# Optimization experiments

Hardware: AMD Instinct MI355X
Metric: run time of the kernel (lower is better)

## Reference

```python
import jax, jax.numpy as jnp
import numpy as np

HEADS = 8

def _flatten(x, s1, s2):
    # 'b c (h s1) (w s2) -> b (h w) (s1 s2 c)'
    b, c, H, W = x.shape
    h, w = H // s1, W // s2
    x = x.reshape(b, c, h, s1, w, s2).transpose(0, 2, 4, 3, 5, 1)
    return x.reshape(b, h * w, s1 * s2 * c)

def _unflatten(x, h, w, s1, s2):
    # 'b (h w) (s1 s2 c) -> b c (h s1) (w s2)'
    b, n, e = x.shape
    c = e // (s1 * s2)
    x = x.reshape(b, h, w, s1, s2, c).transpose(0, 5, 1, 3, 2, 4)
    return x.reshape(b, c, h * s1, w * s2)

def _attn(x_detail, x_context, wq, bq, wk, bk, wv, bv, wo, bo):
    E = x_detail.shape[-1]
    d = E // HEADS
    scale = d ** -0.5
    def split(t):
        b, n, _ = t.shape
        return t.reshape(b, n, HEADS, d).transpose(0, 2, 1, 3)  # b h n d
    q = split(x_context @ wq.T + bq)
    k = split(x_detail @ wk.T + bk)
    v = split(x_detail @ wv.T + bv)
    att = jax.nn.softmax(jnp.einsum('bhqd,bhkd->bhqk', q, k) * scale, axis=-1)
    out = jnp.einsum('bhqk,bhkd->bhqd', att, v)
    b, h, n, _ = out.shape
    out = out.transpose(0, 2, 1, 3).reshape(b, n, E)
    return out @ wo.T + bo

def setup_inputs() -> dict:
    key = jax.random.key(0)
    ks = iter(jax.random.split(key, 64))
    inp = {}
    xshapes = [(16, 96, 56, 56), (16, 192, 28, 28), (16, 384, 14, 14), (16, 768, 7, 7)]
    names = ['x00', 'x10', 'x20', 'x30']
    for nm, sh in zip(names, xshapes):
        inp[nm + '_detail'] = jax.random.normal(next(ks), sh, dtype=jnp.float32)
        inp[nm + '_context'] = jax.random.normal(next(ks), sh, dtype=jnp.float32)
    embs = [384, 192, 384, 768]
    for i, E in enumerate(embs):
        for p in ['q', 'k', 'v', 'o']:
            inp[f'w{p}{i}'] = jax.random.normal(next(ks), (E, E), dtype=jnp.float32) * 0.02
            inp[f'b{p}{i}'] = jnp.zeros((E,), dtype=jnp.float32)
    return inp

def reference(x00_detail, x00_context, x10_detail, x10_context,
              x20_detail, x20_context, x30_detail, x30_context,
              wq0, bq0, wk0, bk0, wv0, bv0, wo0, bo0,
              wq1, bq1, wk1, bk1, wv1, bv1, wo1, bo1,
              wq2, bq2, wk2, bk2, wv2, bv2, wo2, bo2,
              wq3, bq3, wk3, bk3, wv3, bv3, wo3, bo3):
    # scale 0: 56x56 with 2x2 patching -> 784 tokens, emb 384
    o0 = x00_detail + _unflatten(
        _attn(_flatten(x00_detail, 2, 2), _flatten(x00_context, 2, 2),
              wq0, bq0, wk0, bk0, wv0, bv0, wo0, bo0), 28, 28, 2, 2)
    # scale 1: 28x28 -> 784 tokens, emb 192
    o1 = x10_detail + _unflatten(
        _attn(_flatten(x10_detail, 1, 1), _flatten(x10_context, 1, 1),
              wq1, bq1, wk1, bk1, wv1, bv1, wo1, bo1), 28, 28, 1, 1)
    # scale 2: 14x14 -> 196 tokens, emb 384
    o2 = x20_detail + _unflatten(
        _attn(_flatten(x20_detail, 1, 1), _flatten(x20_context, 1, 1),
              wq2, bq2, wk2, bk2, wv2, bv2, wo2, bo2), 14, 14, 1, 1)
    # scale 3: 7x7 -> 49 tokens, emb 768
    o3 = x30_detail + _unflatten(
        _attn(_flatten(x30_detail, 1, 1), _flatten(x30_context, 1, 1),
              wq3, bq3, wk3, bk3, wv3, bv3, wo3, bo3), 7, 7, 1, 1)
    return (o0, o1, o2, o3)
```

## Files before the change

### kernel.cpp

```cpp
#include <hip/hip_runtime.h>
#include <hip/hip_bf16.h>
#include <cstdint>
#include <cstddef>
#include <cmath>

typedef unsigned short bf16u;
typedef float f32x4 __attribute__((ext_vector_type(4)));
typedef short frag8 __attribute__((ext_vector_type(8)));

typedef __attribute__((address_space(1))) uint32_t u32g;
typedef __attribute__((address_space(3))) uint32_t u32l;

__device__ __forceinline__ void async_cp16(const bf16u* g, bf16u* l) {
    __builtin_amdgcn_global_load_lds((u32g*)g, (u32l*)l, 16, 0, 0);
}

__device__ __forceinline__ bf16u f2bf(float f) {
    union { float f; uint32_t u; } v; v.f = f;
    uint32_t u = v.u;
    return (bf16u)((u + 0x7fffu + ((u >> 16) & 1u)) >> 16);
}

__device__ __forceinline__ uint32_t pk2bf(float a, float b) {
    __hip_bfloat162 h = __float22bfloat162_rn(make_float2(a, b));
    union { __hip_bfloat162 h; uint32_t u; } c; c.h = h; return c.u;
}

__device__ __forceinline__ int vperm(int n) {
    return (n & ~63) | ((n & 15) << 2) | ((n >> 4) & 3);
}

static constexpr int cN[4]   = {784, 784, 196, 49};
static constexpr int cE[4]   = {384, 192, 384, 768};
static constexpr int cM[4]   = {12544, 12544, 3136, 784};
static constexpr int cC[4]   = {96, 192, 384, 768};
static constexpr int cH[4]   = {56, 28, 14, 7};
static constexpr int cS[4]   = {2, 1, 1, 1};
static constexpr int cWt[4]  = {28, 28, 14, 7};

static constexpr size_t xoff[4] = {0, 4816896, 7225344, 8429568};
static constexpr size_t voff[4] = {0, 6815744, 10223616, 12320768};
static constexpr size_t woff[4] = {0, 589824, 737280, 1327104};

__device__ __constant__ float qsc[4] = {0.20823509f, 0.29448888f, 0.20823509f, 0.14724444f};

static constexpr int qStart[13] = {0,294,588,882,957,1032,1107,1149,1191,1233,1821,2409,2997};
static constexpr int oStart[5]  = {0,294,369,411,999};

static constexpr int fStart[9] = {0,4800,9600,12000,14400,15744,17088,17856,18624};
static constexpr int wCum[17]  = {0,72,144,216,288,306,324,342,360,432,504,576,648,936,1224,1512,1800};
static constexpr int fNtn[4] = {25, 25, 7, 2};
static constexpr int fNtc[4] = {3, 6, 12, 24};
static constexpr int fSp[4]  = {4, 1, 1, 1};

struct BiasP { const float* p[16]; };
struct PrepP { const float* x[8]; const float* w[16]; };
struct OunfP { const float* xd[4]; };

__global__ __launch_bounds__(256) void prep(PrepP pp, bf16u* __restrict__ Xd,
                                            bf16u* __restrict__ Xc, bf16u* __restrict__ Wb) {
    int blk = blockIdx.x, tid = threadIdx.x;
    if (blk < 18624) {
        __shared__ float tile[32][33];
        int seg = 0;
        while (seg < 7 && blk >= fStart[seg + 1]) seg++;
        int s = seg >> 1, which = seg & 1;
        int l = blk - fStart[seg];
        int ntn = fNtn[s], ntc = fNtc[s], sp = fSp[s];
        int nt = l % ntn; l /= ntn;
        int ctl = l % ntc; l /= ntc;
        int spi = l % sp; int b = l / sp;
        int sv = cS[s];
        int s1i = spi / sv, s2i = spi % sv;
        int C = cC[s], H = cH[s], Wd = cH[s], N = cN[s], E2 = cE[s], Wt = cWt[s];
        const float* x = pp.x[s * 2 + which];
        bf16u* dst = (which ? Xc : Xd) + xoff[s];
        int tx = tid & 31, ty = tid >> 5;
        int n0 = nt * 32, c0 = ctl * 32;
#pragma unroll
        for (int rr = 0; rr < 4; ++rr) {
            int c = c0 + rr * 8 + ty;
            int n = n0 + tx;
            if (n < N) {
                int hh = (n / Wt) * sv + s1i;
                int ww = (n % Wt) * sv + s2i;
                tile[rr * 8 + ty][tx] = x[((size_t)(b * C + c) * H + hh) * Wd + ww];
            }
        }
        __syncthreads();
        int ebase = (s1i * sv + s2i) * C + c0;
#pragma unroll
        for (int rr = 0; rr < 4; ++rr) {
            int n = n0 + rr * 8 + ty;
            if (n < N)
                dst[((size_t)b * N + n) * E2 + ebase + tx] = f2bf(tile[tx][rr * 8 + ty]);
        }
    } else {
        int wb = blk - 18624;
        int m2 = 0;
        while (m2 < 15 && wb >= wCum[m2 + 1]) m2++;
        int s = m2 >> 2, mi = m2 & 3;
        size_t e2 = (size_t)cE[s] * cE[s];
        size_t base = (size_t)(wb - wCum[m2]) * 2048 + tid * 8;
        const float* src = pp.w[m2];
        bf16u* dst = Wb + woff[s] + mi * e2 + base;
        float4 a = *(const float4*)(src + base);
        float4 c = *(const float4*)(src + base + 4);
        bf16u o[8] = {f2bf(a.x), f2bf(a.y), f2bf(a.z), f2bf(a.w),
                      f2bf(c.x), f2bf(c.y), f2bf(c.z), f2bf(c.w)};
        *(frag8*)dst = *(frag8*)o;
    }
}

template<int MODE, int NN, int DHt, int DHPt, int NJt>
__device__ __forceinline__ void gemm_tile128(const bf16u* __restrict__ A, const bf16u* __restrict__ W,
                                             const float* __restrict__ bias,
                                             int M, int E, int mTile, int eTile, float oscale,
                                             bf16u* __restrict__ outB,
                                             bf16u* sm) {
    bf16u* A0 = sm;
    bf16u* B0 = sm + 4096;
    bf16u* A1 = sm + 8192;
    bf16u* B1 = sm + 12288;
    int tid = threadIdx.x, wave = tid >> 6, lane = tid & 63;
    int mbase = mTile * 128, ebase = eTile * 128;
    int wm = (wave & 1) * 64, wn = (wave >> 1) * 64;
    f32x4 acc[4][4] = {};
    int srow = tid >> 2, sch = (tid & 3) * 8;
    int K = E;
    int m0 = mbase + srow;      if (m0 >= M) m0 = M - 1;
    int m1 = mbase + srow + 64; if (m1 >= M) m1 = M - 1;
    const bf16u* Ag0 = A + (size_t)m0 * K + sch;
    const bf16u* Ag1 = A + (size_t)m1 * K + sch;
    const bf16u* Wg0 = W + (size_t)(ebase + srow) * K + sch;
    const bf16u* Wg1 = W + (size_t)(ebase + srow + 64) * K + sch;
    int la = (lane & 15) * 32 + (lane >> 4) * 8;

    auto stage = [&](int k0, bf16u* As, bf16u* Bs) {
        async_cp16(Ag0 + k0, As + tid * 8);
        async_cp16(Ag1 + k0, As + 2048 + tid * 8);
        async_cp16(Wg0 + k0, Bs + tid * 8);
        async_cp16(Wg1 + k0, Bs + 2048 + tid * 8);
    };
    auto compute = [&](const bf16u* As, const bf16u* Bs) {
        frag8 af[4], bfr[4];
#pragma unroll
        for (int i = 0; i < 4; ++i) {
            af[i]  = *(const frag8*)(As + (wm + i * 16) * 32 + la);
            bfr[i] = *(const frag8*)(Bs + (wn + i * 16) * 32 + la);
        }
#pragma unroll
        for (int i = 0; i < 4; ++i)
#pragma unroll
            for (int j = 0; j < 4; ++j)
                acc[i][j] = __builtin_amdgcn_mfma_f32_16x16x32_bf16(af[i], bfr[j], acc[i][j], 0, 0, 0);
    };

    stage(0, A0, B0);
    __syncthreads();
    for (int k0 = 0; k0 < K; k0 += 64) {
        stage(k0 + 32, A1, B1);
        compute(A0, B0);
        __syncthreads();
        if (k0 + 64 < K) stage(k0 + 64, A0, B0);
        compute(A1, B1);
        if (k0 + 64 < K) __syncthreads();
    }

#pragma unroll
    for (int mt = 0; mt < 4; ++mt) {
#pragma unroll
        for (int nt = 0; nt < 4; ++nt) {
            int col = ebase + wn + nt * 16 + (lane & 15);
            float bv = bias[col];
            int rbase = mbase + wm + mt * 16 + (lane >> 4) * 4;
#pragma unroll
            for (int r = 0; r < 4; ++r) {
                int rowg = rbase + r;
                if (rowg >= M) continue;
                float val = (acc[mt][nt][r] + bv) * oscale;
                if (MODE == 0) {
                    outB[(size_t)rowg * E + col] = f2bf(val);
                } else {
                    int bb2 = rowg / NN, n = rowg % NN;
                    int hh = col / DHt, d = col - hh * DHt;
                    outB[((size_t)(bb2 * 8 + hh) * DHPt + d) * NJt + vperm(n)] = f2bf(val);
                }
            }
        }
    }
}

template<int MODE, int NN, int DHt, int DHPt, int NJt>
__device__ __forceinline__ void gemm_tile64(const bf16u* __restrict__ A, const bf16u* __restrict__ W,
                                            const float* __restrict__ bias,
                                            int M, int E, int mTile, int eTile, float oscale,
                                            bf16u* __restrict__ outB,
                                            bf16u* sm) {
    bf16u* A0 = sm;
    bf16u* B0 = sm + 2048;
    bf16u* A1 = sm + 4096;
    bf16u* B1 = sm + 6144;
    int tid = threadIdx.x, wave = tid >> 6, lane = tid & 63;
    int mbase = mTile * 64, ebase = eTile * 64;
    int wm = (wave & 1) * 32, wn = (wave >> 1) * 32;
    f32x4 acc[2][2] = {};
    int srow = tid >> 2, sch = (tid & 3) * 8;
    int K = E;
    int m = mbase + srow; if (m >= M) m = M - 1;
    const bf16u* Ag = A + (size_t)m * K + sch;
    const bf16u* Wg = W + (size_t)(ebase + srow) * K + sch;
    int la = (lane & 15) * 32 + (lane >> 4) * 8;

    auto stage = [&](int k0, bf16u* As, bf16u* Bs) {
        async_cp16(Ag + k0, As + tid * 8);
        async_cp16(Wg + k0, Bs + tid * 8);
    };
    auto compute = [&](const bf16u* As, const bf16u* Bs) {
        frag8 af0 = *(const frag8*)(As + wm * 32 + la);
        frag8 af1 = *(const frag8*)(As + (wm + 16) * 32 + la);
        frag8 bf0 = *(const frag8*)(Bs + wn * 32 + la);
        frag8 bf1 = *(const frag8*)(Bs + (wn + 16) * 32 + la);
        acc[0][0] = __builtin_amdgcn_mfma_f32_16x16x32_bf16(af0, bf0, acc[0][0], 0, 0, 0);
        acc[0][1] = __builtin_amdgcn_mfma_f32_16x16x32_bf16(af0, bf1, acc[0][1], 0, 0, 0);
        acc[1][0] = __builtin_amdgcn_mfma_f32_16x16x32_bf16(af1, bf0, acc[1][0], 0, 0, 0);
        acc[1][1] = __builtin_amdgcn_mfma_f32_16x16x32_bf16(af1, bf1, acc[1][1], 0, 0, 0);
    };

    stage(0, A0, B0);
    __syncthreads();
    for (int k0 = 0; k0 < K; k0 += 64) {
        stage(k0 + 32, A1, B1);
        compute(A0, B0);
        __syncthreads();
        if (k0 + 64 < K) stage(k0 + 64, A0, B0);
        compute(A1, B1);
        if (k0 + 64 < K) __syncthreads();
    }

#pragma unroll
    for (int mt = 0; mt < 2; ++mt) {
#pragma unroll
        for (int nt = 0; nt < 2; ++nt) {
            int col = ebase + wn + nt * 16 + (lane & 15);
            float bv = bias[col];
            int rbase = mbase + wm + mt * 16 + (lane >> 4) * 4;
#pragma unroll
            for (int r = 0; r < 4; ++r) {
                int rowg = rbase + r;
                if (rowg >= M) continue;
                float val = (acc[mt][nt][r] + bv) * oscale;
                if (MODE == 0) {
                    outB[(size_t)rowg * E + col] = f2bf(val);
                } else {
                    int bb2 = rowg / NN, n = rowg % NN;
                    int hh = col / DHt, d = col - hh * DHt;
                    outB[((size_t)(bb2 * 8 + hh) * DHPt + d) * NJt + vperm(n)] = f2bf(val);
                }
            }
        }
    }
}

__global__ __launch_bounds__(256) void qkv_fat(const bf16u* __restrict__ Xd, const bf16u* __restrict__ Xc,
                                               const bf16u* __restrict__ Wb,
                                               bf16u* __restrict__ Qb, bf16u* __restrict__ Kb,
                                               bf16u* __restrict__ Vt, BiasP bp) {
    __shared__ __align__(16) bf16u sm[16384];
    int blk = blockIdx.x;
    int seg = 0;
    while (seg < 11 && blk >= qStart[seg + 1]) seg++;
    int t = blk - qStart[seg];
    if (seg < 9) {
        int s = (seg < 3) ? 0 : (seg < 6 ? 2 : 3);
        int op = seg % 3;
        int E = cE[s], M = cM[s];
        int ct = E >> 7;
        int mTile = t / ct, eTile = t - mTile * ct;
        const bf16u* A = (op == 0 ? Xc : Xd) + xoff[s];
        const bf16u* W = Wb + woff[s] + (size_t)op * E * E;
        const float* bias = bp.p[s * 4 + op];
        if (op == 2) {
            if (s == 0)
                gemm_tile128<1, 784, 48, 64, 832>(A, W, bias, M, E, mTile, eTile, 1.0f, Vt + voff[0], sm);
            else if (s == 2)
                gemm_tile128<1, 196, 48, 64, 256>(A, W, bias, M, E, mTile, eTile, 1.0f, Vt + voff[2], sm);
            else
                gemm_tile128<1, 49, 96, 96, 64>(A, W, bias, M, E, mTile, eTile, 1.0f, Vt + voff[3], sm);
        } else {
            float osc = (op == 0) ? qsc[s] : 1.0f;
            bf16u* outB = (op == 0 ? Qb : Kb) + xoff[s];
            gemm_tile128<0, 0, 1, 0, 0>(A, W, bias, M, E, mTile, eTile, osc, outB, sm);
        }
    } else {
        int op = seg - 9;
        int E = 192, M = 12544;
        int mTile = t / 3, eTile = t - mTile * 3;
        const bf16u* A = (op == 0 ? Xc : Xd) + xoff[1];
        const bf16u* W = Wb + woff[1] + (size_t)op * E * E;
        const float* bias = bp.p[4 + op];
        if (op == 2)
            gemm_tile64<1, 784, 24, 32, 832>(A, W, bias, M, E, mTile, eTile, 1.0f, Vt + voff[1], sm);
        else {
            float osc = (op == 0) ? qsc[1] : 1.0f;
            bf16u* outB = (op == 0 ? Qb : Kb) + xoff[1];
            gemm_tile64<0, 0, 1, 0, 0>(A, W, bias, M, E, mTile, eTile, osc, outB, sm);
        }
    }
}

__device__ __forceinline__ f32x4 bfly_add16(f32x4 v) {
#pragma unroll
    for (int m = 1; m <= 8; m <<= 1) {
        f32x4 o;
#pragma unroll
        for (int e = 0; e < 4; ++e) o[e] = __shfl_xor(v[e], m);
#pragma unroll
        for (int e = 0; e < 4; ++e) v[e] += o[e];
    }
    return v;
}

template<int DH, int N>
__device__ __forceinline__ void attn_body2(bf16u* __restrict__ smem,
                                           const bf16u* __restrict__ Q, const bf16u* __restrict__ K,
                                           const bf16u* __restrict__ Vt, bf16u* __restrict__ O,
                                           int lin) {
    constexpr int DHP = (DH == 24) ? 32 : 64;
    constexpr int C8  = DHP / 8;
    constexpr int CM  = C8 - 1;
    constexpr int KC  = DHP / 32;
    constexpr int DHT = (DH + 15) / 16;
    constexpr int VR  = DHT * 16;
    constexpr int NT  = (N + 63) / 64;
    constexpr int NJc = NT * 64;
    constexpr int E   = DH * 8;
    constexpr int KS  = 64 * C8;
    constexpr int TS  = KS + VR * 8;
    constexpr int RND = (TS + 255) / 256;
    constexpr int PP  = 72;

    bf16u* buf0 = smem;
    bf16u* buf1 = smem + (size_t)TS * 8;
    bf16u* Ps   = smem + (size_t)2 * TS * 8;

    const int qt = lin % NT;
    const int r2 = lin / NT;
    const int h = r2 & 7, b = r2 >> 3;
    const int qb = qt * 64;
    const int tid = threadIdx.x, wave = tid >> 6, lane = tid & 63;
    const int mrow = lane & 15, quad = lane >> 4;

    const bf16u* Kb2 = K + (size_t)b * N * E + h * DH;
    const bf16u* Vb2 = Vt + (size_t)(b * 8 + h) * DHP * NJc;

    auto stage = [&](int jt, bf16u* buf) {
#pragma unroll
        for (int r = 0; r < RND; ++r) {
            int s = tid + r * 256;
            bf16u* dst = buf + (size_t)s * 8;
            if (s < KS) {
                int row = s / C8;
                int cl = (s & CM) ^ (row & CM);
                int n = jt * 64 + row; if (n >= N) n = N - 1;
                async_cp16(Kb2 + (size_t)n * E + cl * 8, dst);
            } else if (s < TS) {
                int v = s - KS;
                int d = v >> 3;
                int cl = (v & 7) ^ (d & 7);
                async_cp16(Vb2 + (size_t)d * NJc + jt * 64 + cl * 8, dst);
            }
        }
    };

    stage(0, buf0);

    frag8 qf[KC];
    {
        int qn = qb + wave * 16 + mrow; if (qn >= N) qn = N - 1;
        const bf16u* qp = Q + (size_t)(b * N + qn) * E + h * DH;
#pragma unroll
        for (int kc = 0; kc < KC; ++kc) {
            int col = kc * 32 + quad * 8;
            frag8 v = {};
            if (col < DH) v = *(const frag8*)(qp + col);
            qf[kc] = v;
        }
    }

    f32x4 lrun = {0.f, 0.f, 0.f, 0.f};
    f32x4 oacc[DHT];
#pragma unroll
    for (int t = 0; t < DHT; ++t) oacc[t] = f32x4{0.f, 0.f, 0.f, 0.f};

    bf16u* Pw = Ps + wave * 16 * PP;

    __syncthreads();

    int p = 0;
    for (int jt = 0; jt < NT; ++jt) {
        bf16u* KsB = p ? buf1 : buf0;
        bf16u* VsB = KsB + (size_t)KS * 8;
        if (jt + 1 < NT) stage(jt + 1, p ? buf0 : buf1);

        f32x4 s[4];
        const bool domask = ((N & 63) != 0) && (jt == NT - 1);
#pragma unroll
        for (int sub = 0; sub < 4; ++sub) {
            f32x4 acc = {};
#pragma unroll
            for (int kc = 0; kc < KC; ++kc) {
                int c = kc * 4 + quad;
                frag8 bfr = *(const frag8*)(KsB + ((size_t)((sub * 16 + mrow) * C8 + (c ^ (mrow & CM)))) * 8);
                acc = __builtin_amdgcn_mfma_f32_16x16x32_bf16(qf[kc], bfr, acc, 0, 0, 0);
            }
            if (domask) {
                int col = jt * 64 + sub * 16 + mrow;
                if (col >= N) { acc[0] = acc[1] = acc[2] = acc[3] = -30000.f; }
            }
            s[sub] = acc;
        }

#pragma unroll
        for (int sub = 0; sub < 4; ++sub)
#pragma unroll
            for (int e = 0; e < 4; ++e) {
                float px = __builtin_amdgcn_exp2f(s[sub][e]);
                s[sub][e] = px;
                lrun[e] += px;
            }

#pragma unroll
        for (int e = 0; e < 4; ++e) {
            uint2 u;
            u.x = pk2bf(s[0][e], s[1][e]);
            u.y = pk2bf(s[2][e], s[3][e]);
            *(uint2*)(Pw + (quad * 4 + e) * PP + mrow * 4) = u;
        }

#pragma unroll
        for (int jc = 0; jc < 2; ++jc) {
            frag8 af = *(const frag8*)(Pw + mrow * PP + jc * 32 + quad * 8);
            int c = jc * 4 + quad;
#pragma unroll
            for (int t = 0; t < DHT; ++t) {
                frag8 bfr = *(const frag8*)(VsB + ((size_t)((t * 16 + mrow) * 8 + (c ^ (mrow & 7)))) * 8);
                oacc[t] = __builtin_amdgcn_mfma_f32_16x16x32_bf16(af, bfr, oacc[t], 0, 0, 0);
            }
        }
        __syncthreads();
        p ^= 1;
    }

    lrun = bfly_add16(lrun);
    f32x4 linv;
#pragma unroll
    for (int e = 0; e < 4; ++e) linv[e] = 1.0f / lrun[e];
#pragma unroll
    for (int t = 0; t < DHT; ++t) {
        int d = t * 16 + mrow;
        if (d >= DH) continue;
#pragma unroll
        for (int e = 0; e < 4; ++e) {
            int n = qb + wave * 16 + quad * 4 + e;
            if (n < N)
                O[((size_t)(b * N + n)) * E + h * DH + d] = f2bf(oacc[t][e] * linv[e]);
        }
    }
}

__global__ __launch_bounds__(256, 4) void attn_fat(const bf16u* __restrict__ Qb, const bf16u* __restrict__ Kb,
                                                   const bf16u* __restrict__ Vt, bf16u* __restrict__ Ob) {
    __shared__ __align__(16) bf16u smem[18944];
    int blk = blockIdx.x;
    if (blk < 1664)
        attn_body2<48, 784>(smem, Qb + xoff[0], Kb + xoff[0], Vt + voff[0], Ob + xoff[0], blk);
    else if (blk < 3328)
        attn_body2<24, 784>(smem, Qb + xoff[1], Kb + xoff[1], Vt + voff[1], Ob + xoff[1], blk - 1664);
    else
        attn_body2<48, 196>(smem, Qb + xoff[2], Kb + xoff[2], Vt + voff[2], Ob + xoff[2], blk - 3328);
}

__global__ __launch_bounds__(256, 2) void attn_s3(const bf16u* __restrict__ Qg, const bf16u* __restrict__ Kg,
                                                  const bf16u* __restrict__ Vtg, bf16u* __restrict__ Og) {
    constexpr int DH = 96, N = 49, DHP = 96, KC = 3, DHT = 6, NJc = 64, E = 768;
    constexpr int KP = 104, QP = 104, VP = 72, PP = 72, C8 = 12;
    __shared__ __align__(16) bf16u smem[20224];
    bf16u* Ks = smem;
    bf16u* Vs = Ks + 64 * KP;
    bf16u* QsPw = Vs + DHT * 16 * VP;

    const bf16u* Q = Qg + xoff[3];
    const bf16u* K = Kg + xoff[3];
    const bf16u* Vt = Vtg + voff[3];
    bf16u* O = Og + xoff[3];

    int lin = blockIdx.x;
    int h = lin & 7, b = lin >> 3;
    int tid = threadIdx.x, wave = tid >> 6, lane = tid & 63;
    int mrow = lane & 15, quad = lane >> 4;

    for (int idx = tid; idx < 64 * C8; idx += 256) {
        int row = idx / C8, col = (idx % C8) * 8;
        int n = row; if (n >= N) n = N - 1;
        frag8 v = {};
        if (col < DH) v = *(const frag8*)(Q + ((size_t)(b * N + n)) * E + h * DH + col);
        *(frag8*)(QsPw + row * QP + col) = v;
    }
    for (int idx = tid; idx < 64 * C8; idx += 256) {
        int row = idx / C8, col = (idx % C8) * 8;
        int n = row; if (n >= N) n = N - 1;
        frag8 v = {};
        if (col < DH) v = *(const frag8*)(K + (size_t)(b * N + n) * E + h * DH + col);
        *(frag8*)(Ks + row * KP + col) = v;
    }
    const bf16u* Vb2 = Vt + (size_t)(b * 8 + h) * DHP * NJc;
    for (int idx = tid; idx < DHT * 16 * 8; idx += 256) {
        int d = idx / 8, j = (idx % 8) * 8;
        frag8 v = {};
        if (d < DH) v = *(const frag8*)(Vb2 + (size_t)d * NJc + j);
        *(frag8*)(Vs + d * VP + j) = v;
    }
    __syncthreads();
    frag8 qf[KC];
#pragma unroll
    for (int kc = 0; kc < KC; ++kc)
        qf[kc] = *(const frag8*)(QsPw + (wave * 16 + mrow) * QP + kc * 32 + quad * 8);
    __syncthreads();
    bf16u* Pw = QsPw + wave * 16 * PP;

    f32x4 lrun = {0.f, 0.f, 0.f, 0.f};
    f32x4 oacc[DHT];
#pragma unroll
    for (int t = 0; t < DHT; ++t) oacc[t] = f32x4{0.f, 0.f, 0.f, 0.f};

    f32x4 s[4];
#pragma unroll
    for (int sub = 0; sub < 4; ++sub) {
        f32x4 acc = {};
#pragma unroll
        for (int kc = 0; kc < KC; ++kc) {
            frag8 bfr = *(const frag8*)(Ks + (sub * 16 + mrow) * KP + kc * 32 + quad * 8);
            acc = __builtin_amdgcn_mfma_f32_16x16x32_bf16(qf[kc], bfr, acc, 0, 0, 0);
        }
        int col = sub * 16 + mrow;
        if (col >= N) { acc[0] = acc[1] = acc[2] = acc[3] = -30000.f; }
        s[sub] = acc;
    }
#pragma unroll
    for (int sub = 0; sub < 4; ++sub)
#pragma unroll
        for (int e = 0; e < 4; ++e) {
            float px = __builtin_amdgcn_exp2f(s[sub][e]);
            s[sub][e] = px;
            lrun[e] += px;
        }
#pragma unroll
    for (int e = 0; e < 4; ++e) {
        uint2 u;
        u.x = pk2bf(s[0][e], s[1][e]);
        u.y = pk2bf(s[2][e], s[3][e]);
        *(uint2*)(Pw + (quad * 4 + e) * PP + mrow * 4) = u;
    }
#pragma unroll
    for (int jc = 0; jc < 2; ++jc) {
        frag8 af = *(const frag8*)(Pw + mrow * PP + jc * 32 + quad * 8);
#pragma unroll
        for (int t = 0; t < DHT; ++t) {
            frag8 bfr = *(const frag8*)(Vs + (t * 16 + mrow) * VP + jc * 32 + quad * 8);
            oacc[t] = __builtin_amdgcn_mfma_f32_16x16x32_bf16(af, bfr, oacc[t], 0, 0, 0);
        }
    }

    lrun = bfly_add16(lrun);
    f32x4 linv;
#pragma unroll
    for (int e = 0; e < 4; ++e) linv[e] = 1.0f / lrun[e];
#pragma unroll
    for (int t = 0; t < DHT; ++t) {
        int d = t * 16 + mrow;
#pragma unroll
        for (int e = 0; e < 4; ++e) {
            int n = wave * 16 + quad * 4 + e;
            if (n < N)
                O[((size_t)(b * N + n)) * E + h * DH + d] = f2bf(oacc[t][e] * linv[e]);
        }
    }
}

template<int SC>
__device__ __forceinline__ size_t out_index(int rowg, int cg) {
    if (SC == 0) {
        int b = rowg / 784, n = rowg - b * 784;
        int slot = cg / 96, c = cg - slot * 96;
        int hh = n / 28, ww = n - hh * 28;
        return ((size_t)(b * 96 + c) * 56 + 2 * hh + (slot >> 1)) * 56 + 2 * ww + (slot & 1);
    } else if (SC == 1) {
        int b = rowg / 784, n = rowg - b * 784;
        return ((size_t)(b * 192 + cg)) * 784 + n;
    } else if (SC == 2) {
        int b = rowg / 196, n = rowg - b * 196;
        return ((size_t)(b * 384 + cg)) * 196 + n;
    } else {
        int b = rowg / 49, n = rowg - b * 49;
        return ((size_t)(b * 768 + cg)) * 49 + n;
    }
}

template<int SC>
__device__ __forceinline__ void o_tile128(const bf16u* __restrict__ A, const bf16u* __restrict__ W,
                                          const float* __restrict__ bias,
                                          const float* __restrict__ xd, float* __restrict__ out,
                                          int M, int E, int mTile, int eTile, bf16u* sm) {
    bf16u* A0 = sm;
    bf16u* B0 = sm + 4096;
    bf16u* A1 = sm + 8192;
    bf16u* B1 = sm + 12288;
    int tid = threadIdx.x, wave = tid >> 6, lane = tid & 63;
    int mbase = mTile * 128, ebase = eTile * 128;
    int wm = (wave & 1) * 64, wn = (wave >> 1) * 64;
    int mrow = lane & 15, quad = lane >> 4;
    f32x4 acc[4][4] = {};
    int srow = tid >> 2, sch = (tid & 3) * 8;
    int K = E;
    int m0 = mbase + srow;      if (m0 >= M) m0 = M - 1;
    int m1 = mbase + srow + 64; if (m1 >= M) m1 = M - 1;
    const bf16u* Ag0 = A + (size_t)m0 * K + sch;
    const bf16u* Ag1 = A + (size_t)m1 * K + sch;
    const bf16u* Wg0 = W + (size_t)(ebase + srow) * K + sch;
    const bf16u* Wg1 = W + (size_t)(ebase + srow + 64) * K + sch;
    int la = mrow * 32 + quad * 8;

    auto stage = [&](int k0, bf16u* As, bf16u* Bs) {
        async_cp16(Ag0 + k0, As + tid * 8);
        async_cp16(Ag1 + k0, As + 2048 + tid * 8);
        async_cp16(Wg0 + k0, Bs + tid * 8);
        async_cp16(Wg1 + k0, Bs + 2048 + tid * 8);
    };
    auto compute = [&](const bf16u* As, const bf16u* Bs) {
        frag8 af[4], bfr[4];
#pragma unroll
        for (int i = 0; i < 4; ++i) {
            af[i]  = *(const frag8*)(As + (wm + i * 16) * 32 + la);
            bfr[i] = *(const frag8*)(Bs + (wn + i * 16) * 32 + la);
        }
#pragma unroll
        for (int i = 0; i < 4; ++i)
#pragma unroll
            for (int j = 0; j < 4; ++j)
                acc[i][j] = __builtin_amdgcn_mfma_f32_16x16x32_bf16(af[i], bfr[j], acc[i][j], 0, 0, 0);
    };

    stage(0, A0, B0);
    __syncthreads();
    for (int k0 = 0; k0 < K; k0 += 64) {
        stage(k0 + 32, A1, B1);
        compute(A0, B0);
        __syncthreads();
        if (k0 + 64 < K) stage(k0 + 64, A0, B0);
        compute(A1, B1);
        if (k0 + 64 < K) __syncthreads();
    }

    float* Ls = (float*)sm;
#pragma unroll
    for (int ph = 0; ph < 4; ++ph) {
        __syncthreads();
        if ((wave & 1) == (ph >> 1)) {
            int mt0 = (ph & 1) * 2;
#pragma unroll
            for (int mi = 0; mi < 2; ++mi) {
                int mt = mt0 + mi;
#pragma unroll
                for (int nt = 0; nt < 4; ++nt)
#pragma unroll
                    for (int r = 0; r < 4; ++r)
                        Ls[(mi * 16 + quad * 4 + r) * 133 + wn + nt * 16 + mrow] = acc[mt][nt][r];
            }
        }
        __syncthreads();
        int rb = mbase + ph * 32;
#pragma unroll
        for (int i = 0; i < 16; ++i) {
            int coll = (tid >> 5) + i * 8;
            int l = tid & 31;
            int rg = rb + l;
            if (rg < M) {
                int cg = ebase + coll;
                size_t oi = out_index<SC>(rg, cg);
                out[oi] = xd[oi] + Ls[l * 133 + coll] + bias[cg];
            }
        }
    }
}

__device__ __forceinline__ void o_tile64_s1(const bf16u* __restrict__ A, const bf16u* __restrict__ W,
                                            const float* __restrict__ bias,
                                            const float* __restrict__ xd, float* __restrict__ out,
                                            int M, int E, int mTile, int eTile, bf16u* sm) {
    bf16u* A0 = sm;
    bf16u* B0 = sm + 2048;
    bf16u* A1 = sm + 4096;
    bf16u* B1 = sm + 6144;
    int tid = threadIdx.x, wave = tid >> 6, lane = tid & 63;
    int mbase = mTile * 64, ebase = eTile * 64;
    int wm = (wave & 1) * 32, wn = (wave >> 1) * 32;
    int mrow = lane & 15, quad = lane >> 4;
    f32x4 acc[2][2] = {};
    int srow = tid >> 2, sch = (tid & 3) * 8;
    int K = E;
    int m = mbase + srow; if (m >= M) m = M - 1;
    const bf16u* Ag = A + (size_t)m * K + sch;
    const bf16u* Wg = W + (size_t)(ebase + srow) * K + sch;
    int la = mrow * 32 + quad * 8;

    auto stage = [&](int k0, bf16u* As, bf16u* Bs) {
        async_cp16(Ag + k0, As + tid * 8);
        async_cp16(Wg + k0, Bs + tid * 8);
    };
    auto compute = [&](const bf16u* As, const bf16u* Bs) {
        frag8 af0 = *(const frag8*)(As + wm * 32 + la);
        frag8 af1 = *(const frag8*)(As + (wm + 16) * 32 + la);
        frag8 bf0 = *(const frag8*)(Bs + wn * 32 + la);
        frag8 bf1 = *(const frag8*)(Bs + (wn + 16) * 32 + la);
        acc[0][0] = __builtin_amdgcn_mfma_f32_16x16x32_bf16(af0, bf0, acc[0][0], 0, 0, 0);
        acc[0][1] = __builtin_amdgcn_mfma_f32_16x16x32_bf16(af0, bf1, acc[0][1], 0, 0, 0);
        acc[1][0] = __builtin_amdgcn_mfma_f32_16x16x32_bf16(af1, bf0, acc[1][0], 0, 0, 0);
        acc[1][1] = __builtin_amdgcn_mfma_f32_16x16x32_bf16(af1, bf1, acc[1][1], 0, 0, 0);
    };

    stage(0, A0, B0);
    __syncthreads();
    for (int k0 = 0; k0 < K; k0 += 64) {
        stage(k0 + 32, A1, B1);
        compute(A0, B0);
        __syncthreads();
        if (k0 + 64 < K) stage(k0 + 64, A0, B0);
        compute(A1, B1);
        if (k0 + 64 < K) __syncthreads();
    }

    float* Ls = (float*)sm;
#pragma unroll
    for (int ph = 0; ph < 2; ++ph) {
        __syncthreads();
        if ((wave & 1) == ph) {
#pragma unroll
            for (int mt = 0; mt < 2; ++mt)
#pragma unroll
                for (int nt = 0; nt < 2; ++nt)
#pragma unroll
                    for (int r = 0; r < 4; ++r)
                        Ls[(mt * 16 + quad * 4 + r) * 69 + wn + nt * 16 + mrow] = acc[mt][nt][r];
        }
        __syncthreads();
        int rb = mbase + ph * 32;
#pragma unroll
        for (int i = 0; i < 8; ++i) {
            int coll = (tid >> 5) + i * 8;
            int l = tid & 31;
            int rg = rb + l;
            if (rg < M) {
                int cg = ebase + coll;
                size_t oi = out_index<1>(rg, cg);
                out[oi] = xd[oi] + Ls[l * 69 + coll] + bias[cg];
            }
        }
    }
}

__global__ __launch_bounds__(256) void ounf_fat(const bf16u* __restrict__ Ob, const bf16u* __restrict__ Wb,
                                                float* __restrict__ out, BiasP bp, OunfP up) {
    __shared__ __align__(16) bf16u sm[16384];
    int blk = blockIdx.x;
    int seg = 0;
    while (seg < 3 && blk >= oStart[seg + 1]) seg++;
    int t = blk - oStart[seg];
    if (seg < 3) {
        int s = (seg == 0) ? 0 : (seg == 1 ? 2 : 3);
        int E = cE[s], M = cM[s];
        int ct = E >> 7;
        int mTile = t / ct, eTile = t - mTile * ct;
        const bf16u* A = Ob + xoff[s];
        const bf16u* W = Wb + woff[s] + (size_t)3 * E * E;
        if (s == 0)
            o_tile128<0>(A, W, bp.p[3], up.xd[0], out + xoff[0], M, E, mTile, eTile, sm);
        else if (s == 2)
            o_tile128<2>(A, W, bp.p[11], up.xd[2], out + xoff[2], M, E, mTile, eTile, sm);
        else
            o_tile128<3>(A, W, bp.p[15], up.xd[3], out + xoff[3], M, E, mTile, eTile, sm);
    } else {
        int E = 192, M = 12544;
        int mTile = t / 3, eTile = t - mTile * 3;
        o_tile64_s1(Ob + xoff[1], Wb + woff[1] + (size_t)3 * E * E, bp.p[7],
                    up.xd[1], out + xoff[1], M, E, mTile, eTile, sm);
    }
}

extern "C" void kernel_launch(void* const* d_in, const int* in_sizes, int n_in,
                              void* d_out, int out_size, void* d_ws, size_t ws_size,
                              hipStream_t stream) {
    bf16u* ws = (bf16u*)d_ws;
    bf16u* Qb = ws;
    bf16u* Kb = ws + 9031680;
    bf16u* Vt = ws + 18063360;
    bf16u* Ob = ws + 31170560;
    bf16u* Wb = ws + 40202240;
    bf16u* Xd = ws + 43888640;
    bf16u* Xc = ws + 52920320;
    float* out = (float*)d_out;

    PrepP pp; BiasP bb; OunfP ux;
    for (int s = 0; s < 4; ++s) {
        pp.x[s * 2]     = (const float*)d_in[s * 2];
        pp.x[s * 2 + 1] = (const float*)d_in[s * 2 + 1];
        ux.xd[s]        = (const float*)d_in[s * 2];
        int w0 = 8 + s * 8;
        pp.w[s * 4 + 0] = (const float*)d_in[w0 + 0];
        pp.w[s * 4 + 1] = (const float*)d_in[w0 + 2];
        pp.w[s * 4 + 2] = (const float*)d_in[w0 + 4];
        pp.w[s * 4 + 3] = (const float*)d_in[w0 + 6];
        bb.p[s * 4 + 0] = (const float*)d_in[w0 + 1];
        bb.p[s * 4 + 1] = (const float*)d_in[w0 + 3];
        bb.p[s * 4 + 2] = (const float*)d_in[w0 + 5];
        bb.p[s * 4 + 3] = (const float*)d_in[w0 + 7];
    }

    prep<<<20424, 256, 0, stream>>>(pp, Xd, Xc, Wb);
    qkv_fat<<<2997, 256, 0, stream>>>(Xd, Xc, Wb, Qb, Kb, Vt, bb);
    attn_fat<<<3840, 256, 0, stream>>>(Qb, Kb, Vt, Ob);
    attn_s3<<<128, 256, 0, stream>>>(Qb, Kb, Vt, Ob);
    ounf_fat<<<999, 256, 0, stream>>>(Ob, Wb, out, bb, ux);
}
```

Baseline: 375.9 us.

## Fuse K and V projections into one GEMM sharing the detail-input tile

Splits the combined QKV launch into a Q-only kernel and a fused K/V kernel. The K/V kernel loads each detail-activation tile once and multiplies it against both Wk and Wv, keeping two accumulator sets. This halves the activation reads for the K and V projections. In exchange it doubles accumulator registers per block, raises LDS use to 48KB, adds a second launch, and caps occupancy at two blocks per CU.

```diff
diff --git a/kernel.cpp b/kernel.cpp
--- a/kernel.cpp
+++ b/kernel.cpp
@@ -44,7 +44,7 @@
 
 __device__ __constant__ float qsc[4] = {0.20823509f, 0.29448888f, 0.20823509f, 0.14724444f};
 
-static constexpr int qStart[13] = {0,294,588,882,957,1032,1107,1149,1191,1233,1821,2409,2997};
+static constexpr int qStartQ[5] = {0, 294, 369, 411, 999};
 static constexpr int oStart[5]  = {0,294,369,411,999};
 
 static constexpr int fStart[9] = {0,4800,9600,12000,14400,15744,17088,17856,18624};
@@ -262,50 +262,221 @@
     }
 }
 
-__global__ __launch_bounds__(256) void qkv_fat(const bf16u* __restrict__ Xd, const bf16u* __restrict__ Xc,
-                                               const bf16u* __restrict__ Wb,
-                                               bf16u* __restrict__ Qb, bf16u* __restrict__ Kb,
-                                               bf16u* __restrict__ Vt, BiasP bp) {
+template<int NN, int DHt, int DHPt, int NJt>
+__device__ __forceinline__ void gemm_kv128(const bf16u* __restrict__ A, const bf16u* __restrict__ Wk,
+                                           const bf16u* __restrict__ Wv,
+                                           const float* __restrict__ bk, const float* __restrict__ bv,
+                                           int M, int E, int mTile, int eTile,
+                                           bf16u* __restrict__ Ko, bf16u* __restrict__ Vo, bf16u* sm) {
+    bf16u* A0 = sm;           bf16u* K0 = sm + 4096;   bf16u* V0 = sm + 8192;
+    bf16u* A1 = sm + 12288;   bf16u* K1 = sm + 16384;  bf16u* V1 = sm + 20480;
+    int tid = threadIdx.x, wave = tid >> 6, lane = tid & 63;
+    int mbase = mTile * 128, ebase = eTile * 128;
+    int wm = (wave & 1) * 64, wn = (wave >> 1) * 64;
+    f32x4 acck[4][4] = {};
+    f32x4 accv[4][4] = {};
+    int srow = tid >> 2, sch = (tid & 3) * 8;
+    int Kd = E;
+    int m0 = mbase + srow;      if (m0 >= M) m0 = M - 1;
+    int m1 = mbase + srow + 64; if (m1 >= M) m1 = M - 1;
+    const bf16u* Ag0 = A + (size_t)m0 * Kd + sch;
+    const bf16u* Ag1 = A + (size_t)m1 * Kd + sch;
+    const bf16u* Kg0 = Wk + (size_t)(ebase + srow) * Kd + sch;
+    const bf16u* Kg1 = Wk + (size_t)(ebase + srow + 64) * Kd + sch;
+    const bf16u* Vg0 = Wv + (size_t)(ebase + srow) * Kd + sch;
+    const bf16u* Vg1 = Wv + (size_t)(ebase + srow + 64) * Kd + sch;
+    int la = (lane & 15) * 32 + (lane >> 4) * 8;
+
+    auto stage = [&](int k0, bf16u* As, bf16u* Ks, bf16u* Vs) {
+        async_cp16(Ag0 + k0, As + tid * 8);
+        async_cp16(Ag1 + k0, As + 2048 + tid * 8);
+        async_cp16(Kg0 + k0, Ks + tid * 8);
+        async_cp16(Kg1 + k0, Ks + 2048 + tid * 8);
+        async_cp16(Vg0 + k0, Vs + tid * 8);
+        async_cp16(Vg1 + k0, Vs + 2048 + tid * 8);
+    };
+    auto compute = [&](const bf16u* As, const bf16u* Ks, const bf16u* Vs) {
+        frag8 af[4], bfr[4];
+#pragma unroll
+        for (int i = 0; i < 4; ++i)
+            af[i] = *(const frag8*)(As + (wm + i * 16) * 32 + la);
+#pragma unroll
+        for (int i = 0; i < 4; ++i)
+            bfr[i] = *(const frag8*)(Ks + (wn + i * 16) * 32 + la);
+#pragma unroll
+        for (int i = 0; i < 4; ++i)
+#pragma unroll
+            for (int j = 0; j < 4; ++j)
+                acck[i][j] = __builtin_amdgcn_mfma_f32_16x16x32_bf16(af[i], bfr[j], acck[i][j], 0, 0, 0);
+#pragma unroll
+        for (int i = 0; i < 4; ++i)
+            bfr[i] = *(const frag8*)(Vs + (wn + i * 16) * 32 + la);
+#pragma unroll
+        for (int i = 0; i < 4; ++i)
+#pragma unroll
+            for (int j = 0; j < 4; ++j)
+                accv[i][j] = __builtin_amdgcn_mfma_f32_16x16x32_bf16(af[i], bfr[j], accv[i][j], 0, 0, 0);
+    };
+
+    stage(0, A0, K0, V0);
+    __syncthreads();
+    for (int k0 = 0; k0 < Kd; k0 += 64) {
+        stage(k0 + 32, A1, K1, V1);
+        compute(A0, K0, V0);
+        __syncthreads();
+        if (k0 + 64 < Kd) stage(k0 + 64, A0, K0, V0);
+        compute(A1, K1, V1);
+        if (k0 + 64 < Kd) __syncthreads();
+    }
+
+#pragma unroll
+    for (int mt = 0; mt < 4; ++mt) {
+#pragma unroll
+        for (int nt = 0; nt < 4; ++nt) {
+            int col = ebase + wn + nt * 16 + (lane & 15);
+            float bkc = bk[col];
+            float bvc = bv[col];
+            int hh = col / DHt, d = col - hh * DHt;
+            int rbase = mbase + wm + mt * 16 + (lane >> 4) * 4;
+#pragma unroll
+            for (int r = 0; r < 4; ++r) {
+                int rowg = rbase + r;
+                if (rowg >= M) continue;
+                Ko[(size_t)rowg * E + col] = f2bf(acck[mt][nt][r] + bkc);
+                int bb2 = rowg / NN, n = rowg % NN;
+                Vo[((size_t)(bb2 * 8 + hh) * DHPt + d) * NJt + vperm(n)] = f2bf(accv[mt][nt][r] + bvc);
+            }
+        }
+    }
+}
+
+template<int NN, int DHt, int DHPt, int NJt>
+__device__ __forceinline__ void gemm_kv64(const bf16u* __restrict__ A, const bf16u* __restrict__ Wk,
+                                          const bf16u* __restrict__ Wv,
+                                          const float* __restrict__ bk, const float* __restrict__ bv,
+                                          int M, int E, int mTile, int eTile,
+                                          bf16u* __restrict__ Ko, bf16u* __restrict__ Vo, bf16u* sm) {
+    bf16u* A0 = sm;          bf16u* K0 = sm + 2048;  bf16u* V0 = sm + 4096;
+    bf16u* A1 = sm + 6144;   bf16u* K1 = sm + 8192;  bf16u* V1 = sm + 10240;
+    int tid = threadIdx.x, wave = tid >> 6, lane = tid & 63;
+    int mbase = mTile * 64, ebase = eTile * 64;
+    int wm = (wave & 1) * 32, wn = (wave >> 1) * 32;
+    f32x4 acck[2][2] = {};
+    f32x4 accv[2][2] = {};
+    int srow = tid >> 2, sch = (tid & 3) * 8;
+    int Kd = E;
+    int m = mbase + srow; if (m >= M) m = M - 1;
+    const bf16u* Ag = A + (size_t)m * Kd + sch;
+    const bf16u* Kg = Wk + (size_t)(ebase + srow) * Kd + sch;
+    const bf16u* Vg = Wv + (size_t)(ebase + srow) * Kd + sch;
+    int la = (lane & 15) * 32 + (lane >> 4) * 8;
+
+    auto stage = [&](int k0, bf16u* As, bf16u* Ks, bf16u* Vs) {
+        async_cp16(Ag + k0, As + tid * 8);
+        async_cp16(Kg + k0, Ks + tid * 8);
+        async_cp16(Vg + k0, Vs + tid * 8);
+    };
+    auto compute = [&](const bf16u* As, const bf16u* Ks, const bf16u* Vs) {
+        frag8 af0 = *(const frag8*)(As + wm * 32 + la);
+        frag8 af1 = *(const frag8*)(As + (wm + 16) * 32 + la);
+        frag8 k0f = *(const frag8*)(Ks + wn * 32 + la);
+        frag8 k1f = *(const frag8*)(Ks + (wn + 16) * 32 + la);
+        acck[0][0] = __builtin_amdgcn_mfma_f32_16x16x32_bf16(af0, k0f, acck[0][0], 0, 0, 0);
+        acck[0][1] = __builtin_amdgcn_mfma_f32_16x16x32_bf16(af0, k1f, acck[0][1], 0, 0, 0);
+        acck[1][0] = __builtin_amdgcn_mfma_f32_16x16x32_bf16(af1, k0f, acck[1][0], 0, 0, 0);
+        acck[1][1] = __builtin_amdgcn_mfma_f32_16x16x32_bf16(af1, k1f, acck[1][1], 0, 0, 0);
+        frag8 v0f = *(const frag8*)(Vs + wn * 32 + la);
+        frag8 v1f = *(const frag8*)(Vs + (wn + 16) * 32 + la);
+        accv[0][0] = __builtin_amdgcn_mfma_f32_16x16x32_bf16(af0, v0f, accv[0][0], 0, 0, 0);
+        accv[0][1] = __builtin_amdgcn_mfma_f32_16x16x32_bf16(af0, v1f, accv[0][1], 0, 0, 0);
+        accv[1][0] = __builtin_amdgcn_mfma_f32_16x16x32_bf16(af1, v0f, accv[1][0], 0, 0, 0);
+        accv[1][1] = __builtin_amdgcn_mfma_f32_16x16x32_bf16(af1, v1f, accv[1][1], 0, 0, 0);
+    };
+
+    stage(0, A0, K0, V0);
+    __syncthreads();
+    for (int k0 = 0; k0 < Kd; k0 += 64) {
+        stage(k0 + 32, A1, K1, V1);
+        compute(A0, K0, V0);
+        __syncthreads();
+        if (k0 + 64 < Kd) stage(k0 + 64, A0, K0, V0);
+        compute(A1, K1, V1);
+        if (k0 + 64 < Kd) __syncthreads();
+    }
+
+#pragma unroll
+    for (int mt = 0; mt < 2; ++mt) {
+#pragma unroll
+        for (int nt = 0; nt < 2; ++nt) {
+            int col = ebase + wn + nt * 16 + (lane & 15);
+            float bkc = bk[col];
+            float bvc = bv[col];
+            int hh = col / DHt, d = col - hh * DHt;
+            int rbase = mbase + wm + mt * 16 + (lane >> 4) * 4;
+#pragma unroll
+            for (int r = 0; r < 4; ++r) {
+                int rowg = rbase + r;
+                if (rowg >= M) continue;
+                Ko[(size_t)rowg * E + col] = f2bf(acck[mt][nt][r] + bkc);
+                int bb2 = rowg / NN, n = rowg % NN;
+                Vo[((size_t)(bb2 * 8 + hh) * DHPt + d) * NJt + vperm(n)] = f2bf(accv[mt][nt][r] + bvc);
+            }
+        }
+    }
+}
+
+__global__ __launch_bounds__(256) void qkv_q(const bf16u* __restrict__ Xc, const bf16u* __restrict__ Wb,
+                                             bf16u* __restrict__ Qb, BiasP bp) {
     __shared__ __align__(16) bf16u sm[16384];
     int blk = blockIdx.x;
     int seg = 0;
-    while (seg < 11 && blk >= qStart[seg + 1]) seg++;
-    int t = blk - qStart[seg];
-    if (seg < 9) {
-        int s = (seg < 3) ? 0 : (seg < 6 ? 2 : 3);
-        int op = seg % 3;
+    while (seg < 3 && blk >= qStartQ[seg + 1]) seg++;
+    int t = blk - qStartQ[seg];
+    if (seg < 3) {
+        int s = (seg == 0) ? 0 : (seg == 1 ? 2 : 3);
         int E = cE[s], M = cM[s];
         int ct = E >> 7;
         int mTile = t / ct, eTile = t - mTile * ct;
-        const bf16u* A = (op == 0 ? Xc : Xd) + xoff[s];
-        const bf16u* W = Wb + woff[s] + (size_t)op * E * E;
-        const float* bias = bp.p[s * 4 + op];
-        if (op == 2) {
-            if (s == 0)
-                gemm_tile128<1, 784, 48, 64, 832>(A, W, bias, M, E, mTile, eTile, 1.0f, Vt + voff[0], sm);
-            else if (s == 2)
-                gemm_tile128<1, 196, 48, 64, 256>(A, W, bias, M, E, mTile, eTile, 1.0f, Vt + voff[2], sm);
-            else
-                gemm_tile128<1, 49, 96, 96, 64>(A, W, bias, M, E, mTile, eTile, 1.0f, Vt + voff[3], sm);
-        } else {
-            float osc = (op == 0) ? qsc[s] : 1.0f;
-            bf16u* outB = (op == 0 ? Qb : Kb) + xoff[s];
-            gemm_tile128<0, 0, 1, 0, 0>(A, W, bias, M, E, mTile, eTile, osc, outB, sm);
-        }
+        gemm_tile128<0, 0, 1, 0, 0>(Xc + xoff[s], Wb + woff[s], bp.p[s * 4], M, E, mTile, eTile,
+                                    qsc[s], Qb + xoff[s], sm);
     } else {
-        int op = seg - 9;
         int E = 192, M = 12544;
         int mTile = t / 3, eTile = t - mTile * 3;
-        const bf16u* A = (op == 0 ? Xc : Xd) + xoff[1];
-        const bf16u* W = Wb + woff[1] + (size_t)op * E * E;
-        const float* bias = bp.p[4 + op];
-        if (op == 2)
-            gemm_tile64<1, 784, 24, 32, 832>(A, W, bias, M, E, mTile, eTile, 1.0f, Vt + voff[1], sm);
-        else {
-            float osc = (op == 0) ? qsc[1] : 1.0f;
-            bf16u* outB = (op == 0 ? Qb : Kb) + xoff[1];
-            gemm_tile64<0, 0, 1, 0, 0>(A, W, bias, M, E, mTile, eTile, osc, outB, sm);
-        }
+        gemm_tile64<0, 0, 1, 0, 0>(Xc + xoff[1], Wb + woff[1], bp.p[4], M, E, mTile, eTile,
+                                   qsc[1], Qb + xoff[1], sm);
+    }
+}
+
+__global__ __launch_bounds__(256, 2) void qkv_kv(const bf16u* __restrict__ Xd, const bf16u* __restrict__ Wb,
+                                                 bf16u* __restrict__ Kb, bf16u* __restrict__ Vt, BiasP bp) {
+    __shared__ __align__(16) bf16u sm[24576];
+    int blk = blockIdx.x;
+    int seg = 0;
+    while (seg < 3 && blk >= qStartQ[seg + 1]) seg++;
+    int t = blk - qStartQ[seg];
+    if (seg < 3) {
+        int s = (seg == 0) ? 0 : (seg == 1 ? 2 : 3);
+        int E = cE[s], M = cM[s];
+        int ct = E >> 7;
+        int mTile = t / ct, eTile = t - mTile * ct;
+        const bf16u* A  = Xd + xoff[s];
+        const bf16u* Wk = Wb + woff[s] + (size_t)1 * E * E;
+        const bf16u* Wv = Wb + woff[s] + (size_t)2 * E * E;
+        if (s == 0)
+            gemm_kv128<784, 48, 64, 832>(A, Wk, Wv, bp.p[1], bp.p[2], M, E, mTile, eTile,
+                                         Kb + xoff[0], Vt + voff[0], sm);
+        else if (s == 2)
+            gemm_kv128<196, 48, 64, 256>(A, Wk, Wv, bp.p[9], bp.p[10], M, E, mTile, eTile,
+                                         Kb + xoff[2], Vt + voff[2], sm);
+        else
+            gemm_kv128<49, 96, 96, 64>(A, Wk, Wv, bp.p[13], bp.p[14], M, E, mTile, eTile,
+                                       Kb + xoff[3], Vt + voff[3], sm);
+    } else {
+        int E = 192, M = 12544;
+        int mTile = t / 3, eTile = t - mTile * 3;
+        gemm_kv64<784, 24, 32, 832>(Xd + xoff[1], Wb + woff[1] + (size_t)1 * E * E,
+                                    Wb + woff[1] + (size_t)2 * E * E, bp.p[5], bp.p[6],
+                                    M, E, mTile, eTile, Kb + xoff[1], Vt + voff[1], sm);
     }
 }
 
@@ -827,7 +998,8 @@
     }
 
     prep<<<20424, 256, 0, stream>>>(pp, Xd, Xc, Wb);
-    qkv_fat<<<2997, 256, 0, stream>>>(Xd, Xc, Wb, Qb, Kb, Vt, bb);
+    qkv_q<<<999, 256, 0, stream>>>(Xc, Wb, Qb, bb);
+    qkv_kv<<<999, 256, 0, stream>>>(Xd, Wb, Kb, Vt, bb);
     attn_fat<<<3840, 256, 0, stream>>>(Qb, Kb, Vt, Ob);
     attn_s3<<<128, 256, 0, stream>>>(Qb, Kb, Vt, Ob);
     ounf_fat<<<999, 256, 0, stream>>>(Ob, Wb, out, bb, ux);
```

New measurement: 384.1 us. 1.02x slower.
